# Performance work log

Measured on AMD Instinct MI355X. Metric: run time of the kernel, lower is better.

## Reference

```python
import jax, jax.numpy as jnp
import numpy as np

EPS_NORM = 1e-5   # instance-norm epsilon (NormalizeLayer over spatial axes)
EPS_VAR = 1e-9    # floor used before sqrt, as in the original


def _instance_norm(x):
    # normalize over spatial axes (1,2), per batch & channel
    mean = jnp.mean(x, axis=(1, 2), keepdims=True)
    var = jnp.var(x, axis=(1, 2), keepdims=True)
    return (x - mean) * jax.lax.rsqrt(var + EPS_NORM)


def _aat(content, style, comb_c, comb_s):
    # content/style: (B,H,W,C); comb_*: (B,H,W,Cc)
    B, H, W, C = content.shape
    N = H * W
    norm_content = _instance_norm(content)
    q = _instance_norm(comb_c).reshape(B, N, -1)   # (B,N,Cc)
    k = _instance_norm(comb_s).reshape(B, N, -1)   # (B,N,Cc)
    v = style.reshape(B, N, C)                     # (B,N,C)
    scores = jnp.einsum('bnc,bmc->bnm', q, k)      # Q_T @ K
    A = jax.nn.softmax(scores, axis=-1)            # (B,N,N)
    M = jnp.einsum('bnm,bmc->bnc', A, v)           # weighted mean
    S2 = jnp.einsum('bnm,bmc->bnc', A, v * v) - M * M  # weighted variance
    S = jnp.sqrt(jnp.maximum(jax.nn.relu(S2), EPS_VAR))
    S = S.reshape(B, H, W, C)
    M = M.reshape(B, H, W, C)
    return S * norm_content + M


def _feature_loss(cs, c, s, cc, sc):
    aat = _aat(c, s, cc, sc)
    return jnp.mean(jnp.square(cs - aat))


def setup_inputs() -> dict:
    key = jax.random.key(0)
    shapes = {
        'cs2': (4, 64, 64, 256), 'c2': (4, 64, 64, 256), 's2': (4, 64, 64, 256),
        'cc2': (4, 64, 64, 448), 'sc2': (4, 64, 64, 448),
        'cs3': (4, 32, 32, 512), 'c3': (4, 32, 32, 512), 's3': (4, 32, 32, 512),
        'cc3': (4, 32, 32, 960), 'sc3': (4, 32, 32, 960),
        'cs4': (4, 16, 16, 512), 'c4': (4, 16, 16, 512), 's4': (4, 16, 16, 512),
        'cc4': (4, 16, 16, 1472), 'sc4': (4, 16, 16, 1472),
    }
    keys = jax.random.split(key, len(shapes))
    return {name: jax.random.normal(k, shp, dtype=jnp.float32)
            for k, (name, shp) in zip(keys, shapes.items())}


def reference(cs2, c2, s2, cc2, sc2, cs3, c3, s3, cc3, sc3, cs4, c4, s4, cc4, sc4):
    loss = _feature_loss(cs2, c2, s2, cc2, sc2)
    loss = loss + _feature_loss(cs3, c3, s3, cc3, sc3)
    loss = loss + _feature_loss(cs4, c4, s4, cc4, sc4)
    return loss
```

## Files before the change

### kernel.cpp

```cpp
#include <hip/hip_runtime.h>
#include <math.h>

#define EPS_NORM 1e-5f
#define EPS_VAR  1e-9f
#define LOG2E    1.4426950408889634f

typedef unsigned short ushort_t;
typedef __attribute__((ext_vector_type(4))) float f32x4;
typedef _Float16 half8 __attribute__((ext_vector_type(8)));

#define MFMAH(a, b, c) __builtin_amdgcn_mfma_f32_16x16x32_f16((a), (b), (c), 0, 0, 0)

#define GLD16(gp, lp) __builtin_amdgcn_global_load_lds(                          \
    (const __attribute__((address_space(1))) unsigned int*)(gp),                 \
    (__attribute__((address_space(3))) unsigned int*)(lp), 16, 0, 0)

__device__ inline ushort_t f16_bits(float x) {
    _Float16 h = (_Float16)x;
    ushort_t u;
    __builtin_memcpy(&u, &h, 2);
    return u;
}
__device__ inline half8 ldh(const ushort_t* p) {
    half8 h;
    __builtin_memcpy(&h, p, 16);
    return h;
}
__device__ inline uint4 pack8(const ushort_t* s) {
    uint4 r;
    r.x = (unsigned)s[0] | ((unsigned)s[1] << 16);
    r.y = (unsigned)s[2] | ((unsigned)s[3] << 16);
    r.z = (unsigned)s[4] | ((unsigned)s[5] << 16);
    r.w = (unsigned)s[6] | ((unsigned)s[7] << 16);
    return r;
}

struct StatJobs {
    const float* x[9];
    float* sm[9];
    float* sq[9];
    int N[9], Cn[9], chG[9], nG[9], base[9];
};
__global__ void __launch_bounds__(256) stat_partial_all(StatJobs J)
{
    int bx = blockIdx.x;
    int j = 0;
#pragma unroll
    for (int k = 1; k < 9; ++k) if (bx >= J.base[k]) j = k;
    bx -= J.base[j];
    const int N = J.N[j], Cn = J.Cn[j], chG = J.chG[j], nG = J.nG[j];
    int b  = bx / (chG * nG);
    int r  = bx % (chG * nG);
    int cg = r / nG;
    int ng = r % nG;
    int ch = cg * 256 + threadIdx.x;
    if (ch >= Cn) return;
    int n0 = ng * 128;
    int n1 = min(n0 + 128, N);
    const float* p = J.x[j] + (long)(b * N) * Cn + ch;
    float s = 0.f, ss = 0.f;
    for (int n = n0; n < n1; ++n) {
        float v = p[(long)n * Cn];
        s += v;
        ss = fmaf(v, v, ss);
    }
    atomicAdd(&J.sm[j][b * Cn + ch], s);
    atomicAdd(&J.sq[j][b * Cn + ch], ss);
}

struct FinJobs {
    float* sm[9];
    float* sq[9];
    int base[9];
    float invN[9];
    int total;
};
__global__ void __launch_bounds__(256) stat_finalize_all(FinJobs J)
{
    int i = blockIdx.x * 256 + threadIdx.x;
    if (i >= J.total) return;
    int j = 0;
#pragma unroll
    for (int k = 1; k < 9; ++k) if (i >= J.base[k]) j = k;
    int e = i - J.base[j];
    float m = J.sm[j][e] * J.invN[j];
    float v = J.sq[j][e] * J.invN[j] - m * m;
    J.sm[j][e] = m;
    J.sq[j][e] = rsqrtf(v + EPS_NORM);
}

__device__ __forceinline__ void norm_quad(
    int bx, const float* __restrict__ qx, const float* __restrict__ qs,
    const float* __restrict__ qq, const float* __restrict__ kx,
    const float* __restrict__ ks, const float* __restrict__ kq,
    ushort_t* __restrict__ qh, ushort_t* __restrict__ kh,
    int N, int Cc, float invN)
{
    const int wave = threadIdx.x >> 6, lane = threadIdx.x & 63;
    int rr = bx * 4 + wave;
    const int BN = 4 * N;
    const bool isQ = rr < BN;
    int bn = isQ ? rr : rr - BN;
    const float* x  = isQ ? qx : kx;
    const float* sm = isQ ? qs : ks;
    const float* sq = isQ ? qq : kq;
    ushort_t* out   = isQ ? qh : kh;
    const float scl = isQ ? LOG2E : 1.0f;
    int b = bn / N;
    long base = (long)bn * Cc;
    const float* smb = sm + b * Cc;
    const float* sqb = sq + b * Cc;
    for (int c8 = lane; c8 * 8 < Cc; c8 += 64) {
        int ch = c8 * 8;
        float4 a0 = *(const float4*)(x + base + ch);
        float4 a1 = *(const float4*)(x + base + ch + 4);
        float4 s0 = *(const float4*)(smb + ch);
        float4 s1 = *(const float4*)(smb + ch + 4);
        float4 t0 = *(const float4*)(sqb + ch);
        float4 t1 = *(const float4*)(sqb + ch + 4);
        ushort_t h8[8];
#pragma unroll
        for (int e = 0; e < 4; ++e) {
            float m = (&s0.x)[e] * invN;
            float r = rsqrtf((&t0.x)[e] * invN - m * m + EPS_NORM);
            h8[e] = f16_bits(((&a0.x)[e] - m) * r * scl);
        }
#pragma unroll
        for (int e = 0; e < 4; ++e) {
            float m = (&s1.x)[e] * invN;
            float r = rsqrtf((&t1.x)[e] * invN - m * m + EPS_NORM);
            h8[4 + e] = f16_bits(((&a1.x)[e] - m) * r * scl);
        }
        *(uint4*)(out + base + ch) = pack8(h8);
    }
}

__device__ __forceinline__ void vtile(
    int bid2, const float* __restrict__ vx, ushort_t* __restrict__ vt,
    int N, int C, ushort_t* tbuf)
{
    const int cT = C >> 6, nT = N >> 6;
    int b   = bid2 / (cT * nT);
    int rem = bid2 % (cT * nT);
    int ch0 = (rem / nT) << 6;
    int n0  = (rem % nT) << 6;
    const int lane = threadIdx.x & 63, wv = threadIdx.x >> 6;
    const float* vb_ = vx + (long)b * N * C + ch0 + lane;
#pragma unroll
    for (int jj = 0; jj < 2; ++jj) {
        int nl = wv * 16 + jj * 8;
        ushort_t h8[8];
#pragma unroll
        for (int i = 0; i < 8; ++i)
            h8[i] = f16_bits(vb_[(long)(n0 + nl + i) * C]);
        *(uint4*)&tbuf[lane * 72 + nl] = pack8(h8);
    }
    __syncthreads();
    {
        const int chl = threadIdx.x >> 2;
        const int nq  = (threadIdx.x & 3) * 16;
        ushort_t* op = vt + ((long)b * C + ch0 + chl) * N + n0 + nq;
        *(uint4*)op       = *(const uint4*)&tbuf[chl * 72 + nq];
        *(uint4*)(op + 8) = *(const uint4*)&tbuf[chl * 72 + nq + 8];
    }
}

__global__ void __launch_bounds__(256) prep2(
    const float* __restrict__ qx, const float* __restrict__ qs, const float* __restrict__ qq,
    const float* __restrict__ kx, const float* __restrict__ ks, const float* __restrict__ kq,
    ushort_t* __restrict__ qh, ushort_t* __restrict__ kh,
    const float* __restrict__ vx, ushort_t* __restrict__ vt)
{
    __shared__ __align__(16) ushort_t lbuf[4608];
    int bx = blockIdx.x;
    if (bx < 8192) norm_quad(bx, qx, qs, qq, kx, ks, kq, qh, kh, 4096, 448, 1.0f / 4096.0f);
    else           vtile(bx - 8192, vx, vt, 4096, 256, lbuf);
}

__device__ inline void stage64_async(const ushort_t* __restrict__ g, long rowBase,
                                     int gstride, int col0, ushort_t* slab, int tid)
{
    const int l  = tid & 63, w = tid >> 6;
    const int rs = l >> 3;
    const int cg = (l & 7) ^ rs;
#pragma unroll
    for (int i = 0; i < 2; ++i) {
        const int r = w * 16 + i * 8 + rs;
        const ushort_t* gp = g + (rowBase + r) * (long)gstride + col0 + (cg << 3);
        ushort_t* lp = slab + (w * 16 + i * 8) * 64 + l * 8;
        GLD16(gp, lp);
    }
}
template<int BROWS>
__device__ inline void stageQ_async(const ushort_t* __restrict__ g, long rowBase,
                                    int gstride, int col0, ushort_t* slab, int tid)
{
    if (tid < BROWS * 8) {
        const int l  = tid & 63, w = tid >> 6;
        const int rs = l >> 3;
        const int cg = (l & 7) ^ rs;
        const int r  = w * 8 + rs;
        const ushort_t* gp = g + (rowBase + r) * (long)gstride + col0 + (cg << 3);
        ushort_t* lp = slab + w * 8 * 64 + l * 8;
        GLD16(gp, lp);
    }
}
__device__ inline half8 ldsw(const ushort_t* slab, int row, int soff)
{
    const int gr = (soff >> 3) ^ (row & 7);
    return ldh(slab + row * 64 + (gr << 3));
}

__global__ void __launch_bounds__(256, 2) flash_pipe(
    const ushort_t* __restrict__ Qh, const ushort_t* __restrict__ Kh,
    const ushort_t* __restrict__ Vth,
    float* __restrict__ Pmo, float* __restrict__ Plo,
    float* __restrict__ PMo, float* __restrict__ PSo)
{
    constexpr int Cc = 448, C = 256, N = 4096, SPLIT = 2;
    constexpr int NKT  = (N / 64) / SPLIT;
    constexpr long VCHO = 64L * N;
    constexpr long KADV = 64L * Cc;

    __shared__ __align__(16) ushort_t smem[4 * 8192 + 4 * 1152];
    const int tid  = threadIdx.x;
    const int lane = tid & 63;
    const int w    = tid >> 6;
    const int l15  = lane & 15;
    const int quad = lane >> 4;

    const int grp = blockIdx.x & 7;
    const int sp  = grp & 1;
    const int b   = grp >> 1;
    const int qb  = (int)(blockIdx.x >> 3);
    const int i0 = qb * 64 + w * 16;
    const long po = (long)(b * (N / 16) + qb * 4 + w) * SPLIT + sp;

    const int rs    = lane >> 3;
    const int cg    = (lane & 7) ^ rs;
    const int ldso0 = w * 1024 + lane * 8;
    const int ldso1 = ldso0 + 512;
    const int xh    = l15 & 7;
    const int lb0   = l15 * 64 + ((quad)     ^ xh) * 8;
    const int lb1   = l15 * 64 + ((4 + quad) ^ xh) * 8;
    ushort_t* const Pw  = smem + 32768 + w * 1152;
    ushort_t* const pww = Pw + quad * 288 + l15;
    const ushort_t* const pfr = Pw + l15 * 72 + quad * 8;

    const long krow0 = (long)b * N + (long)sp * NKT * 64;
    const ushort_t* kp0 = Kh + (krow0 + w * 16 + rs) * (long)Cc + (cg << 3);
    const ushort_t* kp1 = kp0 + 8 * Cc;
    const ushort_t* vp0 = Vth + ((long)b * C + w * 16 + rs) * (long)N
                              + (cg << 3) + (long)sp * NKT * 64;
    const ushort_t* vp1 = vp0 + 8 * (long)N;

#define SLOT(k) (smem + (k) * 8192)
#define STGKP(c0, c1, slot, toff) do {                                           \
    GLD16(kp0 + (toff) + (c0) * 64, SLOT(slot) + ldso0);                         \
    GLD16(kp1 + (toff) + (c0) * 64, SLOT(slot) + ldso1);                         \
    GLD16(kp0 + (toff) + (c1) * 64, SLOT(slot) + 4096 + ldso0);                  \
    GLD16(kp1 + (toff) + (c1) * 64, SLOT(slot) + 4096 + ldso1); } while (0)
#define STGK1(c0, slot, toff) do {                                               \
    GLD16(kp0 + (toff) + (c0) * 64, SLOT(slot) + ldso0);                         \
    GLD16(kp1 + (toff) + (c0) * 64, SLOT(slot) + ldso1); } while (0)
#define STGVP(j0, slot, voff) do {                                               \
    GLD16(vp0 + (voff) + (j0) * VCHO, SLOT(slot) + ldso0);                       \
    GLD16(vp1 + (voff) + (j0) * VCHO, SLOT(slot) + ldso1);                       \
    GLD16(vp0 + (voff) + ((j0) + 1) * VCHO, SLOT(slot) + 4096 + ldso0);          \
    GLD16(vp1 + (voff) + ((j0) + 1) * VCHO, SLOT(slot) + 4096 + ldso1); } while (0)

#define WAITV(NN) asm volatile("s_waitcnt vmcnt(" #NN ")" ::: "memory");         \
    __builtin_amdgcn_sched_barrier(0);                                           \
    __builtin_amdgcn_s_barrier();                                                \
    __builtin_amdgcn_s_setprio(1);
#define PH_END __builtin_amdgcn_s_setprio(0);

#define QKPAIR(slot, c0) do {                                                    \
    const ushort_t* s0_ = SLOT(slot);                                            \
    const ushort_t* s1_ = s0_ + 4096;                                            \
    _Pragma("unroll")                                                            \
    for (int ct = 0; ct < 4; ++ct) S[ct] = MFMAH(qf[2*(c0)+0], ldh(s0_ + ct*1024 + lb0), S[ct]); \
    _Pragma("unroll")                                                            \
    for (int ct = 0; ct < 4; ++ct) S[ct] = MFMAH(qf[2*(c0)+1], ldh(s0_ + ct*1024 + lb1), S[ct]); \
    _Pragma("unroll")                                                            \
    for (int ct = 0; ct < 4; ++ct) S[ct] = MFMAH(qf[2*(c0)+2], ldh(s1_ + ct*1024 + lb0), S[ct]); \
    _Pragma("unroll")                                                            \
    for (int ct = 0; ct < 4; ++ct) S[ct] = MFMAH(qf[2*(c0)+3], ldh(s1_ + ct*1024 + lb1), S[ct]); } while (0)
#define QK1(slot, c0) do {                                                       \
    const ushort_t* s0_ = SLOT(slot);                                            \
    _Pragma("unroll")                                                            \
    for (int ct = 0; ct < 4; ++ct) S[ct] = MFMAH(qf[2*(c0)+0], ldh(s0_ + ct*1024 + lb0), S[ct]); \
    _Pragma("unroll")                                                            \
    for (int ct = 0; ct < 4; ++ct) S[ct] = MFMAH(qf[2*(c0)+1], ldh(s0_ + ct*1024 + lb1), S[ct]); } while (0)
#define PVPAIR(slot, ci0) do {                                                   \
    const ushort_t* s0_ = SLOT(slot);                                            \
    const ushort_t* s1_ = s0_ + 4096;                                            \
    _Pragma("unroll")                                                            \
    for (int ct = 0; ct < 4; ++ct) {                                             \
        half8 vh = ldh(s0_ + ct*1024 + lb0); half8 uh = vh * vh;                 \
        Mac[(ci0)*4 + ct] = MFMAH(pf0, vh, Mac[(ci0)*4 + ct]);                   \
        Sac[(ci0)*4 + ct] = MFMAH(pf0, uh, Sac[(ci0)*4 + ct]); }                 \
    _Pragma("unroll")                                                            \
    for (int ct = 0; ct < 4; ++ct) {                                             \
        half8 vh = ldh(s0_ + ct*1024 + lb1); half8 uh = vh * vh;                 \
        Mac[(ci0)*4 + ct] = MFMAH(pf1, vh, Mac[(ci0)*4 + ct]);                   \
        Sac[(ci0)*4 + ct] = MFMAH(pf1, uh, Sac[(ci0)*4 + ct]); }                 \
    _Pragma("unroll")                                                            \
    for (int ct = 0; ct < 4; ++ct) {                                             \
        half8 vh = ldh(s1_ + ct*1024 + lb0); half8 uh = vh * vh;                 \
        Mac[(ci0+1)*4 + ct] = MFMAH(pf0, vh, Mac[(ci0+1)*4 + ct]);               \
        Sac[(ci0+1)*4 + ct] = MFMAH(pf0, uh, Sac[(ci0+1)*4 + ct]); }             \
    _Pragma("unroll")                                                            \
    for (int ct = 0; ct < 4; ++ct) {                                             \
        half8 vh = ldh(s1_ + ct*1024 + lb1); half8 uh = vh * vh;                 \
        Mac[(ci0+1)*4 + ct] = MFMAH(pf1, vh, Mac[(ci0+1)*4 + ct]);               \
        Sac[(ci0+1)*4 + ct] = MFMAH(pf1, uh, Sac[(ci0+1)*4 + ct]); } } while (0)
#define RESET_S do {                                                             \
// ... 76 lines not shown
        WAITV(8)  QKPAIR(0, 0); PH_END;
        STGK1(6, 3, 0);
        WAITV(6)  QKPAIR(1, 2); PH_END;
        STGVP(0, 0, 0);
        WAITV(6)  QKPAIR(2, 4); PH_END;
        STGVP(2, 1, 0);
        WAITV(8)  QK1(3, 6); PH_END;
        softmax_step();
        STGKP(0, 1, 2, KADV);
        WAITV(8)  PVPAIR(0, 0); PH_END;
        STGKP(2, 3, 3, KADV);
        WAITV(8)  PVPAIR(1, 2); PH_END;

        RESET_S;
        STGKP(4, 5, 0, KADV);
        WAITV(8)  QKPAIR(2, 0); PH_END;
        STGK1(6, 1, KADV);
        WAITV(6)  QKPAIR(3, 2); PH_END;
        STGVP(0, 2, 64);
        WAITV(6)  QKPAIR(0, 4); PH_END;
        STGVP(2, 3, 64);
        WAITV(8)  QK1(1, 6); PH_END;
        softmax_step();
        const bool more = (it + 1 < NKT / 2);
        if (more) {
            kp0 += 2 * KADV; kp1 += 2 * KADV;
            STGKP(0, 1, 0, 0);
            asm volatile("s_waitcnt vmcnt(8)" ::: "memory");
        } else {
            asm volatile("s_waitcnt vmcnt(4)" ::: "memory");
        }
        __builtin_amdgcn_sched_barrier(0);
        __builtin_amdgcn_s_barrier();
        __builtin_amdgcn_s_setprio(1);
        PVPAIR(2, 0);
        PH_END;
        if (more) {
            STGKP(2, 3, 1, 0);
            asm volatile("s_waitcnt vmcnt(8)" ::: "memory");
        } else {
            asm volatile("s_waitcnt vmcnt(0)" ::: "memory");
        }
        __builtin_amdgcn_sched_barrier(0);
        __builtin_amdgcn_s_barrier();
        __builtin_amdgcn_s_setprio(1);
        PVPAIR(3, 2);
        PH_END;

        vp0 += 128; vp1 += 128;
    }
#undef SLOT
#undef STGKP
#undef STGK1
#undef STGVP
#undef WAITV
#undef PH_END
#undef QKPAIR
#undef QK1
#undef PVPAIR
#undef RESET_S

#pragma unroll
    for (int off = 1; off <= 8; off <<= 1)
#pragma unroll
        for (int r = 0; r < 4; ++r) l_l[r] += __shfl_xor(l_l[r], off, 64);

    if (l15 == 0) {
#pragma unroll
        for (int r = 0; r < 4; ++r) {
            Pmo[po * 16 + quad * 4 + r] = m_r[r];
            Plo[po * 16 + quad * 4 + r] = l_l[r];
        }
    }
#pragma unroll
    for (int ct = 0; ct < 16; ++ct)
#pragma unroll
        for (int r = 0; r < 4; ++r) {
            long idx = (po * 16 + quad * 4 + r) * C + ct * 16 + l15;
            PMo[idx] = Mac[ct][r];
            PSo[idx] = Sac[ct][r];
        }
}

template<int Cc, int C, int N, int CSPLIT, bool QREG, int SPLIT, int SLABS, int KGRP>
__device__ __forceinline__ void flash_body(
    const ushort_t* __restrict__ Qh, const ushort_t* __restrict__ Kh,
    const ushort_t* __restrict__ Vth,
    float* __restrict__ Pmo, float* __restrict__ Plo,
    float* __restrict__ PMo, float* __restrict__ PSo,
    ushort_t* smem, int bid)
{
    constexpr int KC      = Cc / 64;
    constexpr int VC      = C / 64;
    constexpr int VCW     = VC / CSPLIT;
    constexpr int CTCW    = 4 * VCW;
    constexpr int STRIPES = 4 / CSPLIT;
    constexpr int BROWS   = 16 * STRIPES;
    constexpr int QB      = N / BROWS;
    constexpr int TILES   = N / 64;
    constexpr int NKT     = TILES / SPLIT;
    constexpr int NKS     = QREG ? (Cc / 32) : 1;
    constexpr int NGRP    = (KC + KGRP - 1) / KGRP;
    constexpr int G       = 4 / CSPLIT;
    constexpr int QCH     = BROWS * 64;
    constexpr int QOFF    = KGRP * 4096;
    constexpr int KQEND   = QOFF + KGRP * QCH;
    constexpr int REGION  = QREG ? (SLABS * 4096)
                                 : (KQEND > SLABS * 4096 ? KQEND : SLABS * 4096);

    const int tid  = threadIdx.x;
    const int lane = tid & 63;
    const int w    = tid >> 6;
    const int l15  = lane & 15;
    const int quad = lane >> 4;

    const int bq = bid / SPLIT;
    const int sp = bid % SPLIT;
    const int b  = bq / QB;
    const int qb = bq % QB;
    const int ls  = w / CSPLIT;
    const int ch2 = w % CSPLIT;
    const int i0 = qb * BROWS + ls * 16;
    const long po = (long)(b * (N / 16) + qb * STRIPES + ls) * SPLIT + sp;
    ushort_t* Pw = smem + REGION + w * 1152;

    half8 qf[NKS];
    if constexpr (QREG) {
        const ushort_t* q1 = Qh + ((long)(b * N + i0 + l15)) * Cc + quad * 8;
#pragma unroll
        for (int ks = 0; ks < NKS; ++ks) qf[ks] = ldh(q1 + ks * 32);
    }

    float m_r[4], l_l[4], mw = -1e30f;
    f32x4 Mac[CTCW], Sac[CTCW];
#pragma unroll
    for (int r = 0; r < 4; ++r) { m_r[r] = -1e30f; l_l[r] = 0.f; }
#pragma unroll
    for (int ct = 0; ct < CTCW; ++ct)
#pragma unroll
        for (int r = 0; r < 4; ++r) { Mac[ct][r] = 0.f; Sac[ct][r] = 0.f; }

    for (int kt = sp * NKT; kt < sp * NKT + NKT; ++kt) {
        const long krow = (long)b * N + kt * 64;

        f32x4 S[4];
#pragma unroll
        for (int ct = 0; ct < 4; ++ct)
#pragma unroll
            for (int r = 0; r < 4; ++r) S[ct][r] = 0.f;

#pragma unroll
        for (int grp = 0; grp < NGRP; ++grp) {
            const int g0 = grp * KGRP;
            const int gn = (KC - g0 < KGRP) ? (KC - g0) : KGRP;
            __syncthreads();
#pragma unroll
            for (int j = 0; j < KGRP; ++j) if (j < gn) {
                stage64_async(Kh, krow, Cc, (g0 + j) * 64, smem + j * 4096, tid);
                if constexpr (!QREG)
                    stageQ_async<BROWS>(Qh, (long)b * N + qb * BROWS, Cc, (g0 + j) * 64,
                                        smem + QOFF + j * QCH, tid);
            }
            __syncthreads();
#pragma unroll
            for (int j = 0; j < KGRP; ++j) if (j < gn) {
                if (((g0 + j) % CSPLIT) == ch2) {
// ... 140 lines not shown
{
    __shared__ __align__(16) ushort_t smem[35328];
    if ((int)blockIdx.x < 512)
        flash_body<960, 512, 1024, 2, false, 4, 5, 5>(
            Qh3, Kh3, Vth3, Pm3, Pl3, PM3, PS3, smem, (int)blockIdx.x);
    else
        flash_body<1472, 512, 256, 4, false, 2, 6, 6>(
            Qh4, Kh4, Vth4, Pm4, Pl4, PM4, PS4, smem, (int)blockIdx.x - 512);
}

template<int C, int SPLIT>
__device__ __forceinline__ void combine_body(
    const float* __restrict__ Pm, const float* __restrict__ Pl,
    const float* __restrict__ PM, const float* __restrict__ PS,
    const float* __restrict__ CT, const float* __restrict__ CS,
    const float* __restrict__ csum, const float* __restrict__ csq,
    float invN, float* __restrict__ loss, int N, int pi, float* shm)
{
    constexpr int CL4 = C / 4;
    float (*wS)[16] = (float(*)[16])shm;
    float* invL = shm + SPLIT * 16;
    float* red  = invL + 16;
    const int nb = N / 16;
    const int b  = pi / nb;
    const long g0 = (long)b * N + (long)(pi % nb) * 16;
    const int tid = threadIdx.x;

    if (tid < 16) {
        float m = -1e30f;
#pragma unroll
        for (int s = 0; s < SPLIT; ++s)
            m = fmaxf(m, Pm[((long)pi * SPLIT + s) * 16 + tid]);
        float L = 0.f;
#pragma unroll
        for (int s = 0; s < SPLIT; ++s) {
            float e = exp2f(Pm[((long)pi * SPLIT + s) * 16 + tid] - m);
            wS[s][tid] = e;
            L = fmaf(e, Pl[((long)pi * SPLIT + s) * 16 + tid], L);
        }
        invL[tid] = 1.f / L;
    }
    __syncthreads();

    float acc = 0.f;
    for (int v = tid; v < 4 * C; v += 256) {
        const int r  = v / CL4;
        const int c0 = (v - r * CL4) * 4;
        const long q0 = (((long)pi * SPLIT) * 16 + r) * C + c0;
        float4 Ms = {0.f, 0.f, 0.f, 0.f}, Ss = {0.f, 0.f, 0.f, 0.f};
#pragma unroll
        for (int s = 0; s < SPLIT; ++s) {
            const float ws_ = wS[s][r];
            const float4 pm = *(const float4*)&PM[q0 + (long)s * 16 * C];
            const float4 ps = *(const float4*)&PS[q0 + (long)s * 16 * C];
            Ms.x = fmaf(ws_, pm.x, Ms.x); Ms.y = fmaf(ws_, pm.y, Ms.y);
            Ms.z = fmaf(ws_, pm.z, Ms.z); Ms.w = fmaf(ws_, pm.w, Ms.w);
            Ss.x = fmaf(ws_, ps.x, Ss.x); Ss.y = fmaf(ws_, ps.y, Ss.y);
            Ss.z = fmaf(ws_, ps.z, Ss.z); Ss.w = fmaf(ws_, ps.w, Ss.w);
        }
        const float iL = invL[r];
        const float4 ctv = *(const float4*)&CT[(g0 + r) * C + c0];
        const float4 csv = *(const float4*)&CS[(g0 + r) * C + c0];
        const float4 cs4 = *(const float4*)&csum[b * C + c0];
        const float4 cq4 = *(const float4*)&csq[b * C + c0];
#pragma unroll
        for (int e = 0; e < 4; ++e) {
            const float Msx = (&Ms.x)[e] * iL;
            const float S2  = (&Ss.x)[e] * iL - Msx * Msx;
            const float Sx  = sqrtf(fmaxf(S2, EPS_VAR));
            const float cm  = (&cs4.x)[e] * invN;
            const float cr  = rsqrtf((&cq4.x)[e] * invN - cm * cm + EPS_NORM);
            const float nc  = ((&ctv.x)[e] - cm) * cr;
            const float d   = (&csv.x)[e] - (Sx * nc + Msx);
            acc = fmaf(d, d, acc);
        }
    }
#pragma unroll
    for (int off = 1; off <= 32; off <<= 1) acc += __shfl_xor(acc, off, 64);
    if ((tid & 63) == 0) red[tid >> 6] = acc;
    __syncthreads();
    if (tid == 0) atomicAdd(loss, red[0] + red[1] + red[2] + red[3]);
}

struct MidP {
    const float *Pm, *Pl, *PM, *PS, *CT, *CS, *csum, *csq;
    float* loss;
    const float *q3x, *q3s, *q3q, *k3x, *k3s, *k3q, *v3x;
    ushort_t *qh3, *kh3, *vt3;
    const float *q4x, *q4s, *q4q, *k4x, *k4s, *k4q, *v4x;
    ushort_t *qh4, *kh4, *vt4;
};
__global__ void __launch_bounds__(256) mid_fused(MidP P)
{
    __shared__ __align__(16) ushort_t lbuf[4608];
    int bx = blockIdx.x;
    if (bx < 1024) {
        combine_body<256, 2>(P.Pm, P.Pl, P.PM, P.PS, P.CT, P.CS, P.csum, P.csq,
                             1.0f / 4096.0f, P.loss, 4096, bx, (float*)lbuf);
    } else if (bx < 3072) {
        norm_quad(bx - 1024, P.q3x, P.q3s, P.q3q, P.k3x, P.k3s, P.k3q,
                  P.qh3, P.kh3, 1024, 960, 1.0f / 1024.0f);
    } else if (bx < 3584) {
        vtile(bx - 3072, P.v3x, P.vt3, 1024, 512, lbuf);
    } else if (bx < 4096) {
        norm_quad(bx - 3584, P.q4x, P.q4s, P.q4q, P.k4x, P.k4s, P.k4q,
                  P.qh4, P.kh4, 256, 1472, 1.0f / 256.0f);
    } else {
        vtile(bx - 4096, P.v4x, P.vt4, 256, 512, lbuf);
    }
}

struct C34P {
    const float *Pm3, *Pl3, *PM3, *PS3, *CT3, *CS3, *c3s, *c3q;
    const float *Pm4, *Pl4, *PM4, *PS4, *CT4, *CS4, *c4s, *c4q;
    float* lossp;
    float* out;
    float s0, s1, s2;
};
__global__ void __launch_bounds__(256) combine34_final(C34P P)
{
    __shared__ float shm[4 * 16 + 20];
    int bx = blockIdx.x;
    if (bx < 256)
        combine_body<512, 4>(P.Pm3, P.Pl3, P.PM3, P.PS3, P.CT3, P.CS3, P.c3s, P.c3q,
                             1.0f / 1024.0f, &P.lossp[1], 1024, bx, shm);
    else
        combine_body<512, 2>(P.Pm4, P.Pl4, P.PM4, P.PS4, P.CT4, P.CS4, P.c4s, P.c4q,
                             1.0f / 256.0f, &P.lossp[2], 256, bx - 256, shm);
    __threadfence();
    if (threadIdx.x == 0) {
        unsigned old = atomicAdd((unsigned*)&P.lossp[3], 1u);
        if (old == 319u) {
            float l0 = atomicAdd(&P.lossp[0], 0.0f);
            float l1 = atomicAdd(&P.lossp[1], 0.0f);
            float l2 = atomicAdd(&P.lossp[2], 0.0f);
            P.out[0] = l0 * P.s0 + l1 * P.s1 + l2 * P.s2;
        }
    }
}

template<int CCL, int CL, int NQ>
__global__ void __launch_bounds__(256) flash_aat(
    const float* __restrict__ Q, const float* __restrict__ K, const float* __restrict__ V,
    const float* __restrict__ CT, const float* __restrict__ CS,
    const float* __restrict__ qmean, const float* __restrict__ qrstd,
    const float* __restrict__ kmean, const float* __restrict__ krstd,
    const float* __restrict__ cmean, const float* __restrict__ crstd,
    float* __restrict__ loss, int N)
{
    constexpr int CC   = CCL * 64;
    constexpr int C    = CL * 64;
    constexpr int ROWS = 4 * NQ;
    const int lane = threadIdx.x & 63;
    const int wave = threadIdx.x >> 6;
    const int rowBlocks = N / ROWS;
    const int b  = blockIdx.x / rowBlocks;
    const int rb = blockIdx.x % rowBlocks;
    const int i0 = rb * ROWS + wave * NQ;

    float kmu[CCL], krs[CCL];
#pragma unroll
    for (int t = 0; t < CCL; ++t) {
        int ch = lane + 64 * t;
        kmu[t] = kmean[b * CC + ch];
        krs[t] = krstd[b * CC + ch];
    }
// ... 51 lines not shown
                float pv = p * vv[t];
                Macc[qi][t] += pv;
                Sacc[qi][t] = fmaf(pv, vv[t], Sacc[qi][t]);
            }
        }
    }
    float acc = 0.f;
#pragma unroll
    for (int qi = 0; qi < NQ; ++qi) {
        float inv_l = 1.f / lsum[qi];
        long base = (long)(b * N + i0 + qi) * C;
#pragma unroll
        for (int t = 0; t < CL; ++t) {
            int ch = lane + 64 * t;
            float M  = Macc[qi][t] * inv_l;
            float S2 = Sacc[qi][t] * inv_l - M * M;
            float S  = sqrtf(fmaxf(S2, EPS_VAR));
            float nc = (CT[base + ch] - cmean[b * C + ch]) * crstd[b * C + ch];
            float d  = CS[base + ch] - (S * nc + M);
            acc = fmaf(d, d, acc);
        }
    }
#pragma unroll
    for (int off = 32; off > 0; off >>= 1) acc += __shfl_xor(acc, off, 64);
    if (lane == 0) atomicAdd(loss, acc);
}

__global__ void combine_loss(const float* __restrict__ lp, float* __restrict__ out,
                             float s0, float s1, float s2)
{
    out[0] = lp[0] * s0 + lp[1] * s1 + lp[2] * s2;
}

extern "C" void kernel_launch(void* const* d_in, const int* in_sizes, int n_in,
                              void* d_out, int out_size, void* d_ws, size_t ws_size,
                              hipStream_t stream)
{
    const float* cs2 = (const float*)d_in[0];
    const float* c2  = (const float*)d_in[1];
    const float* s2v = (const float*)d_in[2];
    const float* cc2 = (const float*)d_in[3];
    const float* sc2 = (const float*)d_in[4];
    const float* cs3 = (const float*)d_in[5];
    const float* c3  = (const float*)d_in[6];
    const float* s3v = (const float*)d_in[7];
    const float* cc3 = (const float*)d_in[8];
    const float* sc3 = (const float*)d_in[9];
    const float* cs4 = (const float*)d_in[10];
    const float* c4  = (const float*)d_in[11];
    const float* s4v = (const float*)d_in[12];
    const float* cc4 = (const float*)d_in[13];
    const float* sc4 = (const float*)d_in[14];

    const int B = 4;
    float* ws = (float*)d_ws;
    size_t fo = 0;
    auto allocF = [&](size_t n) { float* p = ws + fo; fo += n; return p; };

    float* lossp = allocF(4);
    float* c2m = allocF(B * 256);  float* c2r = allocF(B * 256);
    float* q2m = allocF(B * 448);  float* q2r = allocF(B * 448);
    float* k2m = allocF(B * 448);  float* k2r = allocF(B * 448);
    float* c3m = allocF(B * 512);  float* c3r = allocF(B * 512);
    float* q3m = allocF(B * 960);  float* q3r = allocF(B * 960);
    float* k3m = allocF(B * 960);  float* k3r = allocF(B * 960);
    float* c4m = allocF(B * 512);  float* c4r = allocF(B * 512);
    float* q4m = allocF(B * 1472); float* q4r = allocF(B * 1472);
    float* k4m = allocF(B * 1472); float* k4r = allocF(B * 1472);
    size_t zeroBytes = fo * sizeof(float);

    float* Pm = allocF(32768);
    float* Pl = allocF(32768);
    float* PM = allocF(8388608);
    float* PS = allocF(8388608);

    size_t arenaOff = ((fo * 4 + 15) & ~(size_t)15) / 2;
    ushort_t* arena = (ushort_t*)d_ws + arenaOff;
    const size_t arenaShorts = 18874400;
    size_t need = arenaOff * 2 + arenaShorts * 2;
    const bool fast = (ws_size >= need);

    hipMemsetAsync(d_ws, 0, zeroBytes, stream);

    {
        StatJobs SJ;
        const float* xs[9] = {c2, cc2, sc2, c3, cc3, sc3, c4, cc4, sc4};
        float* sms[9] = {c2m, q2m, k2m, c3m, q3m, k3m, c4m, q4m, k4m};
        float* sqs[9] = {c2r, q2r, k2r, c3r, q3r, k3r, c4r, q4r, k4r};
        const int Ns[9]  = {4096, 4096, 4096, 1024, 1024, 1024, 256, 256, 256};
        const int Cns[9] = {256, 448, 448, 512, 960, 960, 512, 1472, 1472};
        int pb = 0;
        for (int j = 0; j < 9; ++j) {
            int chG = (Cns[j] + 255) / 256;
            int nG  = (Ns[j] + 127) / 128;
            SJ.x[j] = xs[j]; SJ.sm[j] = sms[j]; SJ.sq[j] = sqs[j];
            SJ.N[j] = Ns[j]; SJ.Cn[j] = Cns[j]; SJ.chG[j] = chG; SJ.nG[j] = nG;
            SJ.base[j] = pb;
            pb += B * chG * nG;
        }
        hipLaunchKernelGGL(stat_partial_all, dim3(pb), dim3(256), 0, stream, SJ);
    }

    if (fast) {
        ushort_t* qh2 = arena;
        ushort_t* kh2 = qh2 + (size_t)B * 4096 * 448;
        ushort_t* vh2 = kh2 + (size_t)B * 4096 * 448;
        ushort_t* qh3 = arena;
        ushort_t* kh3 = qh3 + (size_t)B * 1024 * 960;
        ushort_t* vh3 = kh3 + (size_t)B * 1024 * 960;
        ushort_t* qh4 = vh3 + (size_t)B * 1024 * 512;
        ushort_t* kh4 = qh4 + (size_t)B * 256 * 1472;
        ushort_t* vh4 = kh4 + (size_t)B * 256 * 1472;
        size_t o34 = (size_t)B * 1024 * 960 * 2 + (size_t)B * 1024 * 512
                   + (size_t)B * 256 * 1472 * 2 + (size_t)B * 256 * 512;
        float* PM4 = (float*)(arena + o34);
        float* PS4 = PM4 + 1048576;
        float* Pm4 = Pm + 16384;
        float* Pl4 = Pl + 16384;

        hipLaunchKernelGGL(prep2, dim3(8192 + 1024), dim3(256), 0, stream,
                           cc2, q2m, q2r, sc2, k2m, k2r, qh2, kh2, s2v, vh2);
        hipLaunchKernelGGL(flash_pipe, dim3(512), dim3(256), 0, stream,
                           qh2, kh2, vh2, Pm, Pl, PM, PS);
        {
            MidP MP;
            MP.Pm = Pm; MP.Pl = Pl; MP.PM = PM; MP.PS = PS;
            MP.CT = c2; MP.CS = cs2; MP.csum = c2m; MP.csq = c2r;
            MP.loss = &lossp[0];
            MP.q3x = cc3; MP.q3s = q3m; MP.q3q = q3r;
            MP.k3x = sc3; MP.k3s = k3m; MP.k3q = k3r; MP.v3x = s3v;
            MP.qh3 = qh3; MP.kh3 = kh3; MP.vt3 = vh3;
            MP.q4x = cc4; MP.q4s = q4m; MP.q4q = q4r;
            MP.k4x = sc4; MP.k4s = k4m; MP.k4q = k4r; MP.v4x = s4v;
            MP.qh4 = qh4; MP.kh4 = kh4; MP.vt4 = vh4;
            hipLaunchKernelGGL(mid_fused, dim3(4224), dim3(256), 0, stream, MP);
        }
        hipLaunchKernelGGL(flash34, dim3(512 + 128), dim3(256), 0, stream,
                           qh3, kh3, vh3, Pm, Pl, PM, PS,
                           qh4, kh4, vh4, Pm4, Pl4, PM4, PS4);
        {
            C34P CP;
            CP.Pm3 = Pm; CP.Pl3 = Pl; CP.PM3 = PM; CP.PS3 = PS;
            CP.CT3 = c3; CP.CS3 = cs3; CP.c3s = c3m; CP.c3q = c3r;
            CP.Pm4 = Pm4; CP.Pl4 = Pl4; CP.PM4 = PM4; CP.PS4 = PS4;
            CP.CT4 = c4; CP.CS4 = cs4; CP.c4s = c4m; CP.c4q = c4r;
            CP.lossp = lossp; CP.out = (float*)d_out;
            CP.s0 = 1.0f / (4.0f * 4096.0f * 256.0f);
            CP.s1 = 1.0f / (4.0f * 1024.0f * 512.0f);
            CP.s2 = 1.0f / (4.0f * 256.0f * 512.0f);
            hipLaunchKernelGGL(combine34_final, dim3(256 + 64), dim3(256), 0, stream, CP);
        }
    } else {
        {
            FinJobs FJ;
            float* sms[9] = {c2m, q2m, k2m, c3m, q3m, k3m, c4m, q4m, k4m};
            float* sqs[9] = {c2r, q2r, k2r, c3r, q3r, k3r, c4r, q4r, k4r};
            const int Ns[9]  = {4096, 4096, 4096, 1024, 1024, 1024, 256, 256, 256};
            const int Cns[9] = {256, 448, 448, 512, 960, 960, 512, 1472, 1472};
            int fb = 0;
            for (int j = 0; j < 9; ++j) {
                FJ.sm[j] = sms[j]; FJ.sq[j] = sqs[j]; FJ.base[j] = fb;
                FJ.invN[j] = 1.0f / (float)Ns[j];
                fb += B * Cns[j];
            }
            FJ.total = fb;
            hipLaunchKernelGGL(stat_finalize_all, dim3((fb + 255) / 256), dim3(256), 0, stream, FJ);
        }
        hipLaunchKernelGGL((flash_aat<7, 4, 4>), dim3(B * 4096 / 16), dim3(256), 0, stream,
                           cc2, sc2, s2v, c2, cs2, q2m, q2r, k2m, k2r, c2m, c2r, &lossp[0], 4096);
        hipLaunchKernelGGL((flash_aat<15, 8, 2>), dim3(B * 1024 / 8), dim3(256), 0, stream,
                           cc3, sc3, s3v, c3, cs3, q3m, q3r, k3m, k3r, c3m, c3r, &lossp[1], 1024);
        hipLaunchKernelGGL((flash_aat<23, 8, 2>), dim3(B * 256 / 8), dim3(256), 0, stream,
                           cc4, sc4, s4v, c4, cs4, q4m, q4r, k4m, k4r, c4m, c4r, &lossp[2], 256);
        hipLaunchKernelGGL(combine_loss, dim3(1), dim3(1), 0, stream,
                           lossp, (float*)d_out,
                           1.0f / (4.0f * 4096.0f * 256.0f),
                           1.0f / (4.0f * 1024.0f * 512.0f),
                           1.0f / (4.0f * 256.0f * 512.0f));
    }
}
```

Baseline: 650.3 us.

## Fuse all pipeline stages into one cooperative persistent kernel with grid syncs

Replaces the sequence of separate launches (stats, prep, flash, mid, flash34, combine) with one cooperative kernel of 512 blocks that walks through the stages with grid-wide barriers between them. It also vectorises the statistics pass to float4 loads with four-row-group warps. The aim is to remove launch gaps and tail effects between the stages. In exchange, every stage is now limited to 512 resident blocks, which may lower parallelism for the memory-bound phases, and grid.sync adds its own cost. The old multi-kernel path is kept as a fallback if the cooperative launch fails.

```diff
diff --git a/kernel.cpp b/kernel.cpp
--- a/kernel.cpp
+++ b/kernel.cpp
@@ -1,5 +1,8 @@
 #include <hip/hip_runtime.h>
+#include <hip/hip_cooperative_groups.h>
 #include <math.h>
+
+namespace cg = cooperative_groups;
 
 #define EPS_NORM 1e-5f
 #define EPS_VAR  1e-9f
@@ -35,37 +38,51 @@
     return r;
 }
 
-struct StatJobs {
+struct StatJobs4 {
     const float* x[9];
     float* sm[9];
     float* sq[9];
-    int N[9], Cn[9], chG[9], nG[9], base[9];
+    int N[9], Cn[9], cG[9], nG[9], base[9];
 };
-__global__ void __launch_bounds__(256) stat_partial_all(StatJobs J)
-{
-    int bx = blockIdx.x;
+__device__ __forceinline__ void stat_body(const StatJobs4& J, int bx)
+{
     int j = 0;
 #pragma unroll
     for (int k = 1; k < 9; ++k) if (bx >= J.base[k]) j = k;
     bx -= J.base[j];
-    const int N = J.N[j], Cn = J.Cn[j], chG = J.chG[j], nG = J.nG[j];
-    int b  = bx / (chG * nG);
-    int r  = bx % (chG * nG);
-    int cg = r / nG;
-    int ng = r % nG;
-    int ch = cg * 256 + threadIdx.x;
-    if (ch >= Cn) return;
-    int n0 = ng * 128;
-    int n1 = min(n0 + 128, N);
-    const float* p = J.x[j] + (long)(b * N) * Cn + ch;
-    float s = 0.f, ss = 0.f;
+    const int N = J.N[j], Cn = J.Cn[j], cG = J.cG[j], nG = J.nG[j];
+    const int b   = bx / (cG * nG);
+    const int r   = bx % (cG * nG);
+    const int cgi = r / nG;
+    const int ng  = r % nG;
+    const int lane = threadIdx.x & 63, wv = threadIdx.x >> 6;
+    const int c4 = cgi * 64 + lane;
+    if (c4 * 4 >= Cn) return;
+    const int n0 = ng * 128 + wv * 32;
+    if (n0 >= N) return;
+    const int n1 = min(n0 + 32, N);
+    const int c4s = Cn >> 2;
+    const float4* p = (const float4*)(J.x[j] + (long)(b * N) * Cn) + (long)n0 * c4s + c4;
+    float4 s  = {0.f, 0.f, 0.f, 0.f};
+    float4 ss = {0.f, 0.f, 0.f, 0.f};
     for (int n = n0; n < n1; ++n) {
-        float v = p[(long)n * Cn];
-        s += v;
-        ss = fmaf(v, v, ss);
-    }
-    atomicAdd(&J.sm[j][b * Cn + ch], s);
-    atomicAdd(&J.sq[j][b * Cn + ch], ss);
+        float4 v = *p;
+        p += c4s;
+        s.x += v.x; s.y += v.y; s.z += v.z; s.w += v.w;
+        ss.x = fmaf(v.x, v.x, ss.x); ss.y = fmaf(v.y, v.y, ss.y);
+        ss.z = fmaf(v.z, v.z, ss.z); ss.w = fmaf(v.w, v.w, ss.w);
+    }
+    float* smp = J.sm[j] + b * Cn + c4 * 4;
+    float* sqp = J.sq[j] + b * Cn + c4 * 4;
+#pragma unroll
+    for (int e = 0; e < 4; ++e) {
+        atomicAdd(&smp[e], (&s.x)[e]);
+        atomicAdd(&sqp[e], (&ss.x)[e]);
+    }
+}
+__global__ void __launch_bounds__(256) stat_partial_all(StatJobs4 J)
+{
+    stat_body(J, (int)blockIdx.x);
 }
 
 struct FinJobs {
@@ -165,18 +182,6 @@
     }
 }
 
-__global__ void __launch_bounds__(256) prep2(
-    const float* __restrict__ qx, const float* __restrict__ qs, const float* __restrict__ qq,
-    const float* __restrict__ kx, const float* __restrict__ ks, const float* __restrict__ kq,
-    ushort_t* __restrict__ qh, ushort_t* __restrict__ kh,
-    const float* __restrict__ vx, ushort_t* __restrict__ vt)
-{
-    __shared__ __align__(16) ushort_t lbuf[4608];
-    int bx = blockIdx.x;
-    if (bx < 8192) norm_quad(bx, qx, qs, qq, kx, ks, kq, qh, kh, 4096, 448, 1.0f / 4096.0f);
-    else           vtile(bx - 8192, vx, vt, 4096, 256, lbuf);
-}
-
 __device__ inline void stage64_async(const ushort_t* __restrict__ g, long rowBase,
                                      int gstride, int col0, ushort_t* slab, int tid)
 {
@@ -211,28 +216,28 @@
     return ldh(slab + row * 64 + (gr << 3));
 }
 
-__global__ void __launch_bounds__(256, 2) flash_pipe(
+__device__ __forceinline__ void flash2_body(
     const ushort_t* __restrict__ Qh, const ushort_t* __restrict__ Kh,
     const ushort_t* __restrict__ Vth,
     float* __restrict__ Pmo, float* __restrict__ Plo,
-    float* __restrict__ PMo, float* __restrict__ PSo)
+    float* __restrict__ PMo, float* __restrict__ PSo,
+    ushort_t* smem, int bid)
 {
     constexpr int Cc = 448, C = 256, N = 4096, SPLIT = 2;
     constexpr int NKT  = (N / 64) / SPLIT;
     constexpr long VCHO = 64L * N;
     constexpr long KADV = 64L * Cc;
 
-    __shared__ __align__(16) ushort_t smem[4 * 8192 + 4 * 1152];
     const int tid  = threadIdx.x;
     const int lane = tid & 63;
     const int w    = tid >> 6;
     const int l15  = lane & 15;
     const int quad = lane >> 4;
 
-    const int grp = blockIdx.x & 7;
+    const int grp = bid & 7;
     const int sp  = grp & 1;
     const int b   = grp >> 1;
-    const int qb  = (int)(blockIdx.x >> 3);
+    const int qb  = bid >> 3;
     const int i0 = qb * 64 + w * 16;
     const long po = (long)(b * (N / 16) + qb * 4 + w) * SPLIT + sp;
 
@@ -475,6 +480,16 @@
         }
 }
 
+__global__ void __launch_bounds__(256, 2) flash_pipe(
+    const ushort_t* __restrict__ Qh, const ushort_t* __restrict__ Kh,
+    const ushort_t* __restrict__ Vth,
+    float* __restrict__ Pmo, float* __restrict__ Plo,
+    float* __restrict__ PMo, float* __restrict__ PSo)
+{
+    __shared__ __align__(16) ushort_t smem[37376];
+    flash2_body(Qh, Kh, Vth, Pmo, Plo, PMo, PSo, smem, (int)blockIdx.x);
+}
+
 template<int Cc, int C, int N, int CSPLIT, bool QREG, int SPLIT, int SLABS, int KGRP>
 __device__ __forceinline__ void flash_body(
     const ushort_t* __restrict__ Qh, const ushort_t* __restrict__ Kh,
@@ -781,6 +796,114 @@
     if (tid == 0) atomicAdd(loss, red[0] + red[1] + red[2] + red[3]);
 }
 
+struct MegaP {
+    StatJobs4 SJ; int statBlocks;
+    const float *cc2, *sc2, *s2v;
+    const float *q2m, *q2r, *k2m, *k2r;
+    ushort_t *qh2, *kh2, *vh2;
+    float *Pm, *Pl, *PM, *PS;
+    const float *c2, *cs2, *c2m, *c2r;
+    float* lossp;
+    const float *cc3, *sc3, *s3v, *q3m, *q3r, *k3m, *k3r;
+    ushort_t *qh3, *kh3, *vh3;
+    const float *cc4, *sc4, *s4v, *q4m, *q4r, *k4m, *k4r;
+    ushort_t *qh4, *kh4, *vh4;
+    float *Pm4, *Pl4, *PM4, *PS4;
+    const float *c3, *cs3, *c3m, *c3r, *c4, *cs4, *c4m, *c4r;
+    float* out;
+    float s0, s1, s2;
+};
+
+__global__ void __launch_bounds__(256, 2) mega(MegaP P)
+{
+    __shared__ __align__(16) ushort_t smem[37376];
+    cg::grid_group grid = cg::this_grid();
+    const int nb  = (int)gridDim.x;
+    const int bid = (int)blockIdx.x;
+
+    for (int v = bid; v < P.statBlocks; v += nb) stat_body(P.SJ, v);
+    __threadfence();
+    grid.sync();
+
+    for (int v = bid; v < 9216; v += nb) {
+        if (v < 8192)
+            norm_quad(v, P.cc2, P.q2m, P.q2r, P.sc2, P.k2m, P.k2r,
+                      P.qh2, P.kh2, 4096, 448, 1.0f / 4096.0f);
+        else
+            vtile(v - 8192, P.s2v, P.vh2, 4096, 256, smem);
+        __syncthreads();
+    }
+    __threadfence();
+    grid.sync();
+
+    flash2_body(P.qh2, P.kh2, P.vh2, P.Pm, P.Pl, P.PM, P.PS, smem, bid);
+    __threadfence();
+    grid.sync();
+
+    for (int v = bid; v < 4224; v += nb) {
+        if (v < 1024)
+            combine_body<256, 2>(P.Pm, P.Pl, P.PM, P.PS, P.c2, P.cs2, P.c2m, P.c2r,
+                                 1.0f / 4096.0f, &P.lossp[0], 4096, v, (float*)smem);
+        else if (v < 3072)
+            norm_quad(v - 1024, P.cc3, P.q3m, P.q3r, P.sc3, P.k3m, P.k3r,
+                      P.qh3, P.kh3, 1024, 960, 1.0f / 1024.0f);
+        else if (v < 3584)
+            vtile(v - 3072, P.s3v, P.vh3, 1024, 512, smem);
+        else if (v < 4096)
+            norm_quad(v - 3584, P.cc4, P.q4m, P.q4r, P.sc4, P.k4m, P.k4r,
+                      P.qh4, P.kh4, 256, 1472, 1.0f / 256.0f);
+        else
+            vtile(v - 4096, P.s4v, P.vh4, 256, 512, smem);
+        __syncthreads();
+    }
+    __threadfence();
+    grid.sync();
+
+    for (int v = bid; v < 640; v += nb) {
+        if (v < 512)
+            flash_body<960, 512, 1024, 2, false, 4, 5, 5>(
+                P.qh3, P.kh3, P.vh3, P.Pm, P.Pl, P.PM, P.PS, smem, v);
+        else
+            flash_body<1472, 512, 256, 4, false, 2, 6, 6>(
+                P.qh4, P.kh4, P.vh4, P.Pm4, P.Pl4, P.PM4, P.PS4, smem, v - 512);
+        __syncthreads();
+    }
+    __threadfence();
+    grid.sync();
+
+    for (int v = bid; v < 320; v += nb) {
+        if (v < 256)
+            combine_body<512, 4>(P.Pm, P.Pl, P.PM, P.PS, P.c3, P.cs3, P.c3m, P.c3r,
+                                 1.0f / 1024.0f, &P.lossp[1], 1024, v, (float*)smem);
+        else
+            combine_body<512, 2>(P.Pm4, P.Pl4, P.PM4, P.PS4, P.c4, P.cs4, P.c4m, P.c4r,
+                                 1.0f / 256.0f, &P.lossp[2], 256, v - 256, (float*)smem);
+        __threadfence();
+        if (threadIdx.x == 0) {
+            unsigned old = atomicAdd((unsigned*)&P.lossp[3], 1u);
+            if (old == 319u) {
+                float l0 = atomicAdd(&P.lossp[0], 0.0f);
+                float l1 = atomicAdd(&P.lossp[1], 0.0f);
+                float l2 = atomicAdd(&P.lossp[2], 0.0f);
+                P.out[0] = l0 * P.s0 + l1 * P.s1 + l2 * P.s2;
+            }
+        }
+        __syncthreads();
+    }
+}
+
+__global__ void __launch_bounds__(256) prep2(
+    const float* __restrict__ qx, const float* __restrict__ qs, const float* __restrict__ qq,
+    const float* __restrict__ kx, const float* __restrict__ ks, const float* __restrict__ kq,
+    ushort_t* __restrict__ qh, ushort_t* __restrict__ kh,
+    const float* __restrict__ vx, ushort_t* __restrict__ vt)
+{
+    __shared__ __align__(16) ushort_t lbuf[4608];
+    int bx = blockIdx.x;
+    if (bx < 8192) norm_quad(bx, qx, qs, qq, kx, ks, kq, qh, kh, 4096, 448, 1.0f / 4096.0f);
+    else           vtile(bx - 8192, vx, vt, 4096, 256, lbuf);
+}
+
 struct MidP {
     const float *Pm, *Pl, *PM, *PS, *CT, *CS, *csum, *csq;
     float* loss;
@@ -998,23 +1121,22 @@
 
     hipMemsetAsync(d_ws, 0, zeroBytes, stream);
 
+    StatJobs4 SJ;
+    int statBlocks = 0;
     {
-        StatJobs SJ;
         const float* xs[9] = {c2, cc2, sc2, c3, cc3, sc3, c4, cc4, sc4};
         float* sms[9] = {c2m, q2m, k2m, c3m, q3m, k3m, c4m, q4m, k4m};
         float* sqs[9] = {c2r, q2r, k2r, c3r, q3r, k3r, c4r, q4r, k4r};
         const int Ns[9]  = {4096, 4096, 4096, 1024, 1024, 1024, 256, 256, 256};
         const int Cns[9] = {256, 448, 448, 512, 960, 960, 512, 1472, 1472};
-        int pb = 0;
         for (int j = 0; j < 9; ++j) {
-            int chG = (Cns[j] + 255) / 256;
-            int nG  = (Ns[j] + 127) / 128;
+            int cG = (Cns[j] + 255) / 256;
+            int nG = (Ns[j] + 127) / 128;
             SJ.x[j] = xs[j]; SJ.sm[j] = sms[j]; SJ.sq[j] = sqs[j];
-            SJ.N[j] = Ns[j]; SJ.Cn[j] = Cns[j]; SJ.chG[j] = chG; SJ.nG[j] = nG;
-            SJ.base[j] = pb;
-            pb += B * chG * nG;
-        }
-        hipLaunchKernelGGL(stat_partial_all, dim3(pb), dim3(256), 0, stream, SJ);
+            SJ.N[j] = Ns[j]; SJ.Cn[j] = Cns[j]; SJ.cG[j] = cG; SJ.nG[j] = nG;
+            SJ.base[j] = statBlocks;
+            statBlocks += B * cG * nG;
+        }
     }
 
     if (fast) {
@@ -1034,39 +1156,69 @@
         float* Pm4 = Pm + 16384;
         float* Pl4 = Pl + 16384;
 
-        hipLaunchKernelGGL(prep2, dim3(8192 + 1024), dim3(256), 0, stream,
-                           cc2, q2m, q2r, sc2, k2m, k2r, qh2, kh2, s2v, vh2);
-        hipLaunchKernelGGL(flash_pipe, dim3(512), dim3(256), 0, stream,
-                           qh2, kh2, vh2, Pm, Pl, PM, PS);
-        {
-            MidP MP;
-            MP.Pm = Pm; MP.Pl = Pl; MP.PM = PM; MP.PS = PS;
-            MP.CT = c2; MP.CS = cs2; MP.csum = c2m; MP.csq = c2r;
-            MP.loss = &lossp[0];
-            MP.q3x = cc3; MP.q3s = q3m; MP.q3q = q3r;
-            MP.k3x = sc3; MP.k3s = k3m; MP.k3q = k3r; MP.v3x = s3v;
-            MP.qh3 = qh3; MP.kh3 = kh3; MP.vt3 = vh3;
-            MP.q4x = cc4; MP.q4s = q4m; MP.q4q = q4r;
-            MP.k4x = sc4; MP.k4s = k4m; MP.k4q = k4r; MP.v4x = s4v;
-            MP.qh4 = qh4; MP.kh4 = kh4; MP.vt4 = vh4;
-            hipLaunchKernelGGL(mid_fused, dim3(4224), dim3(256), 0, stream, MP);
-        }
-        hipLaunchKernelGGL(flash34, dim3(512 + 128), dim3(256), 0, stream,
-                           qh3, kh3, vh3, Pm, Pl, PM, PS,
-                           qh4, kh4, vh4, Pm4, Pl4, PM4, PS4);
-        {
-            C34P CP;
-            CP.Pm3 = Pm; CP.Pl3 = Pl; CP.PM3 = PM; CP.PS3 = PS;
-            CP.CT3 = c3; CP.CS3 = cs3; CP.c3s = c3m; CP.c3q = c3r;
-            CP.Pm4 = Pm4; CP.Pl4 = Pl4; CP.PM4 = PM4; CP.PS4 = PS4;
-            CP.CT4 = c4; CP.CS4 = cs4; CP.c4s = c4m; CP.c4q = c4r;
-            CP.lossp = lossp; CP.out = (float*)d_out;
-            CP.s0 = 1.0f / (4.0f * 4096.0f * 256.0f);
-            CP.s1 = 1.0f / (4.0f * 1024.0f * 512.0f);
-            CP.s2 = 1.0f / (4.0f * 256.0f * 512.0f);
-            hipLaunchKernelGGL(combine34_final, dim3(256 + 64), dim3(256), 0, stream, CP);
+        MegaP MP;
+        MP.SJ = SJ; MP.statBlocks = statBlocks;
+        MP.cc2 = cc2; MP.sc2 = sc2; MP.s2v = s2v;
+        MP.q2m = q2m; MP.q2r = q2r; MP.k2m = k2m; MP.k2r = k2r;
+        MP.qh2 = qh2; MP.kh2 = kh2; MP.vh2 = vh2;
+        MP.Pm = Pm; MP.Pl = Pl; MP.PM = PM; MP.PS = PS;
+        MP.c2 = c2; MP.cs2 = cs2; MP.c2m = c2m; MP.c2r = c2r;
+        MP.lossp = lossp;
+        MP.cc3 = cc3; MP.sc3 = sc3; MP.s3v = s3v;
+        MP.q3m = q3m; MP.q3r = q3r; MP.k3m = k3m; MP.k3r = k3r;
+        MP.qh3 = qh3; MP.kh3 = kh3; MP.vh3 = vh3;
+        MP.cc4 = cc4; MP.sc4 = sc4; MP.s4v = s4v;
+        MP.q4m = q4m; MP.q4r = q4r; MP.k4m = k4m; MP.k4r = k4r;
+        MP.qh4 = qh4; MP.kh4 = kh4; MP.vh4 = vh4;
+        MP.Pm4 = Pm4; MP.Pl4 = Pl4; MP.PM4 = PM4; MP.PS4 = PS4;
+        MP.c3 = c3; MP.cs3 = cs3; MP.c3m = c3m; MP.c3r = c3r;
+        MP.c4 = c4; MP.cs4 = cs4; MP.c4m = c4m; MP.c4r = c4r;
+        MP.out = (float*)d_out;
+        MP.s0 = 1.0f / (4.0f * 4096.0f * 256.0f);
+        MP.s1 = 1.0f / (4.0f * 1024.0f * 512.0f);
+        MP.s2 = 1.0f / (4.0f * 256.0f * 512.0f);
+
+        void* args[] = { (void*)&MP };
+        hipError_t er = hipLaunchCooperativeKernel(
+            reinterpret_cast<void*>(mega), dim3(512), dim3(256), args, 0, stream);
+
+        if (er != hipSuccess) {
+            hipLaunchKernelGGL(stat_partial_all, dim3(statBlocks), dim3(256), 0, stream, SJ);
+            hipLaunchKernelGGL(prep2, dim3(8192 + 1024), dim3(256), 0, stream,
+                               cc2, q2m, q2r, sc2, k2m, k2r, qh2, kh2, s2v, vh2);
+            hipLaunchKernelGGL(flash_pipe, dim3(512), dim3(256), 0, stream,
+                               qh2, kh2, vh2, Pm, Pl, PM, PS);
+            {
+                MidP MDP;
+                MDP.Pm = Pm; MDP.Pl = Pl; MDP.PM = PM; MDP.PS = PS;
+                MDP.CT = c2; MDP.CS = cs2; MDP.csum = c2m; MDP.csq = c2r;
+                MDP.loss = &lossp[0];
+                MDP.q3x = cc3; MDP.q3s = q3m; MDP.q3q = q3r;
+                MDP.k3x = sc3; MDP.k3s = k3m; MDP.k3q = k3r; MDP.v3x = s3v;
+                MDP.qh3 = qh3; MDP.kh3 = kh3; MDP.vt3 = vh3;
+                MDP.q4x = cc4; MDP.q4s = q4m; MDP.q4q = q4r;
+                MDP.k4x = sc4; MDP.k4s = k4m; MDP.k4q = k4r; MDP.v4x = s4v;
+                MDP.qh4 = qh4; MDP.kh4 = kh4; MDP.vt4 = vh4;
+                hipLaunchKernelGGL(mid_fused, dim3(4224), dim3(256), 0, stream, MDP);
+            }
+            hipLaunchKernelGGL(flash34, dim3(512 + 128), dim3(256), 0, stream,
+                               qh3, kh3, vh3, Pm, Pl, PM, PS,
+                               qh4, kh4, vh4, Pm4, Pl4, PM4, PS4);
+            {
+                C34P CP;
+                CP.Pm3 = Pm; CP.Pl3 = Pl; CP.PM3 = PM; CP.PS3 = PS;
+                CP.CT3 = c3; CP.CS3 = cs3; CP.c3s = c3m; CP.c3q = c3r;
+                CP.Pm4 = Pm4; CP.Pl4 = Pl4; CP.PM4 = PM4; CP.PS4 = PS4;
+                CP.CT4 = c4; CP.CS4 = cs4; CP.c4s = c4m; CP.c4q = c4r;
+                CP.lossp = lossp; CP.out = (float*)d_out;
+                CP.s0 = 1.0f / (4.0f * 4096.0f * 256.0f);
+                CP.s1 = 1.0f / (4.0f * 1024.0f * 512.0f);
+                CP.s2 = 1.0f / (4.0f * 256.0f * 512.0f);
+                hipLaunchKernelGGL(combine34_final, dim3(256 + 64), dim3(256), 0, stream, CP);
+            }
         }
     } else {
+        hipLaunchKernelGGL(stat_partial_all, dim3(statBlocks), dim3(256), 0, stream, SJ);
         {
             FinJobs FJ;
             float* sms[9] = {c2m, q2m, k2m, c3m, q3m, k3m, c4m, q4m, k4m};
```

New measurement: 1.369 ms. +110.6%, slower.
